# Kernel optimization log

Measured on AMD Instinct MI355X. Metric: run time of the kernel, lower is better.

The kernel has to match this reference:

```python
import jax, jax.numpy as jnp
import numpy as np

N = 100000      # nodes
E = 1600000     # edges
F_IN = 128      # node feature dim
F_E = 16        # edge feature dim
H = 4           # heads
C = 32          # per-head channels
NEG_SLOPE = 0.2


def setup_inputs() -> dict:
    key = jax.random.key(0)
    ks = jax.random.split(key, 8)
    s = 0.05
    x = jax.random.normal(ks[0], (N, F_IN), jnp.float32)
    edge_index = jax.random.randint(ks[1], (2, E), 0, N, jnp.int32)
    edge_attr = jax.random.normal(ks[2], (E, F_E), jnp.float32)
    Wl = jax.random.normal(ks[3], (F_IN, H * C), jnp.float32) * s   # lin_l (source)
    Wr = jax.random.normal(ks[4], (F_IN, H * C), jnp.float32) * s   # lin_r (target)
    We = jax.random.normal(ks[5], (F_E, H * C), jnp.float32) * s    # lin_edge
    att = jax.random.normal(ks[6], (H, C), jnp.float32) * s         # attention vector a
    bias = jnp.zeros((H * C,), jnp.float32)
    return {"x": x, "edge_index": edge_index, "edge_attr": edge_attr,
            "Wl": Wl, "Wr": Wr, "We": We, "att": att, "bias": bias}


def reference(x, edge_index, edge_attr, Wl, Wr, We, att, bias):
    n = x.shape[0]
    src, dst = edge_index[0], edge_index[1]

    # add_self_loops=True, fill_value='mean': self-loop edge_attr of node i is the
    # mean of edge_attr of edges whose destination is i (0 if no incoming edges).
    ea_sum = jax.ops.segment_sum(edge_attr, dst, num_segments=n)            # [n, Fe]
    cnt = jax.ops.segment_sum(jnp.ones((edge_attr.shape[0], 1), edge_attr.dtype),
                              dst, num_segments=n)                          # [n, 1]
    loop_attr = ea_sum / jnp.maximum(cnt, 1.0)
    loop = jnp.arange(n, dtype=src.dtype)
    src2 = jnp.concatenate([src, loop])                                     # [E+n]
    dst2 = jnp.concatenate([dst, loop])
    ea2 = jnp.concatenate([edge_attr, loop_attr], axis=0)                   # [E+n, Fe]

    # GATv2: score_e = att . leaky_relu(Wl x_src + Wr x_dst + We e)
    xl = (x @ Wl).reshape(n, H, C)
    xr = (x @ Wr).reshape(n, H, C)
    ee = (ea2 @ We).reshape(-1, H, C)
    e = jax.nn.leaky_relu(xl[src2] + xr[dst2] + ee, NEG_SLOPE)              # [E+n, H, C]
    logit = jnp.einsum('ehc,hc->eh', e, att)                                # [E+n, H]

    # segment softmax over destination node (self-loops guarantee nonempty segments)
    m = jax.ops.segment_max(logit, dst2, num_segments=n)                    # [n, H]
    ev = jnp.exp(logit - m[dst2])
    denom = jax.ops.segment_sum(ev, dst2, num_segments=n)
    alpha = ev / denom[dst2]                                                # [E+n, H]

    # scatter-aggregate weighted source messages
    out = jax.ops.segment_sum(alpha[:, :, None] * xl[src2], dst2, num_segments=n)
    out = out.reshape(n, H * C) + bias
    return jax.nn.relu(out), alpha
```

## Files before the change

kernel.cpp:

```cpp
#include <hip/hip_runtime.h>
#include <hip/hip_bf16.h>

#define HC   128
#define FE   16
#define NEG  0.2f
#define SPAD 140

using bf16 = __hip_bfloat16;
using f16  = _Float16;
typedef _Float16 h2 __attribute__((ext_vector_type(2)));
typedef short s16x8 __attribute__((ext_vector_type(8)));
typedef float f32x4 __attribute__((ext_vector_type(4)));

static __device__ __forceinline__ size_t szt(int a) { return (size_t)a; }
static __device__ __forceinline__ short b16rne(float f) {
    unsigned u = __float_as_uint(f);
    unsigned r = (u + 0x7fffu + ((u >> 16) & 1u)) >> 16;
    return (short)r;
}
static __device__ __forceinline__ unsigned pkh(float x, float y) {
    auto h = __builtin_amdgcn_cvt_pkrtz(x, y);
    return __builtin_bit_cast(unsigned, h);
}
static __device__ __forceinline__ float hlo(unsigned u) {
    h2 v = __builtin_bit_cast(h2, u); return (float)v.x;
}
static __device__ __forceinline__ float hhi(unsigned u) {
    h2 v = __builtin_bit_cast(h2, u); return (float)v.y;
}
static __device__ __forceinline__ float dot2(h2 a, h2 b, float c) {
#if __has_builtin(__builtin_amdgcn_fdot2)
    return __builtin_amdgcn_fdot2(a, b, c, false);
#else
    return c + (float)a.x * (float)b.x + (float)a.y * (float)b.y;
#endif
}
static __device__ __forceinline__ int xcc_id() {
    int x;
    asm volatile("s_getreg_b32 %0, hwreg(HW_REG_XCC_ID)" : "=s"(x));
    return x & 7;
}


__global__ void k_rank(const int* __restrict__ dst, int* __restrict__ cnt2,
                       int* __restrict__ rank, int E) {
    int g = xcc_id();
    int base = (blockIdx.x * 256 + threadIdx.x) * 4;
    if (base >= E) return;
    unsigned gtag = (unsigned)g << 28;
    if (base + 3 < E) {
        int4 d4 = *reinterpret_cast<const int4*>(dst + base);
        int r0 = __hip_atomic_fetch_add(&cnt2[d4.x * 8 + g], 1, __ATOMIC_RELAXED,
                                        __HIP_MEMORY_SCOPE_WORKGROUP);
        int r1 = __hip_atomic_fetch_add(&cnt2[d4.y * 8 + g], 1, __ATOMIC_RELAXED,
                                        __HIP_MEMORY_SCOPE_WORKGROUP);
        int r2 = __hip_atomic_fetch_add(&cnt2[d4.z * 8 + g], 1, __ATOMIC_RELAXED,
                                        __HIP_MEMORY_SCOPE_WORKGROUP);
        int r3 = __hip_atomic_fetch_add(&cnt2[d4.w * 8 + g], 1, __ATOMIC_RELAXED,
                                        __HIP_MEMORY_SCOPE_WORKGROUP);
        *reinterpret_cast<int4*>(rank + base) =
            make_int4(r0 | gtag, r1 | gtag, r2 | gtag, r3 | gtag);
    } else {
        for (int e = base; e < E; ++e) {
            int r = __hip_atomic_fetch_add(&cnt2[dst[e] * 8 + g], 1, __ATOMIC_RELAXED,
                                           __HIP_MEMORY_SCOPE_WORKGROUP);
            rank[e] = r | gtag;
        }
    }
}

__global__ __launch_bounds__(1024) void k_scan1(const int* __restrict__ cnt,
                                                int* __restrict__ excl,
                                                int* __restrict__ bsum, int n) {
    __shared__ int wsum[16];
    int t = threadIdx.x, lane = t & 63, wv = t >> 6;
    int i = blockIdx.x * 4096 + t * 4;
    int4 c = make_int4(0, 0, 0, 0);
    if (i + 3 < n) c = *reinterpret_cast<const int4*>(&cnt[i]);
    else if (i < n) {
        c.x = cnt[i];
        c.y = (i + 1 < n) ? cnt[i + 1] : 0;
        c.z = (i + 2 < n) ? cnt[i + 2] : 0;
    }
    int tot = c.x + c.y + c.z + c.w;
    int s = tot;
    #pragma unroll
    for (int d = 1; d < 64; d <<= 1) { int u = __shfl_up(s, d); if (lane >= d) s += u; }
    if (lane == 63) wsum[wv] = s;
    __syncthreads();
    if (t < 16) {
        int ws = wsum[t];
        #pragma unroll
        for (int d = 1; d < 16; d <<= 1) { int u = __shfl_up(ws, d); if (t >= d) ws += u; }
        wsum[t] = ws;
    }
    __syncthreads();
    int excl_t = (wv ? wsum[wv - 1] : 0) + (s - tot);
    if (i < n) {
        int4 ro;
        ro.x = excl_t;
        ro.y = ro.x + c.x;
        ro.z = ro.y + c.y;
        ro.w = ro.z + c.z;
        if (i + 3 < n) *reinterpret_cast<int4*>(&excl[i]) = ro;
        else {
            excl[i] = ro.x;
            if (i + 1 < n) excl[i + 1] = ro.y;
            if (i + 2 < n) excl[i + 2] = ro.z;
        }
    }
    if (t == 0) bsum[blockIdx.x] = wsum[15];
}

__global__ void k_scan2(int* __restrict__ bsum, int nb) {
    int t = threadIdx.x;
    int carry = 0;
    for (int base = 0; base < nb; base += 64) {
        int i = base + t;
        int v = (i < nb) ? bsum[i] : 0;
        int s = v;
        #pragma unroll
        for (int d = 1; d < 64; d <<= 1) { int u = __shfl_up(s, d); if (t >= d) s += u; }
        if (i < nb) bsum[i] = carry + s - v;
        carry += __shfl(s, 63);
    }
}

__global__ void k_scan3(const int* __restrict__ bsum, int* __restrict__ off2,
                        int* __restrict__ row_off, int n8, int E) {
    int i = blockIdx.x * 256 + threadIdx.x;
    if (i < n8) {
        int v = off2[i] + bsum[i >> 12];
        off2[i] = v;
        if ((i & 7) == 0) row_off[i >> 3] = v;
    } else if (i == n8) {
        row_off[n8 >> 3] = E;
    }
}

__global__ void k_fill(const int* __restrict__ src, const int* __restrict__ dst,
                       const int* __restrict__ rank, const int* __restrict__ off2,
                       int4* __restrict__ pairs4, int E) {
    int base = (blockIdx.x * 256 + threadIdx.x) * 4;
    if (base >= E) return;
    if (base + 3 < E) {
        int4 d4 = *reinterpret_cast<const int4*>(dst + base);
        int4 s4 = *reinterpret_cast<const int4*>(src + base);
        int4 k4 = *reinterpret_cast<const int4*>(rank + base);
        int p0 = off2[d4.x * 8 + (((unsigned)k4.x) >> 28)] + (k4.x & 0x0FFFFFFF);
        int p1 = off2[d4.y * 8 + (((unsigned)k4.y) >> 28)] + (k4.y & 0x0FFFFFFF);
        int p2 = off2[d4.z * 8 + (((unsigned)k4.z) >> 28)] + (k4.z & 0x0FFFFFFF);
        int p3 = off2[d4.w * 8 + (((unsigned)k4.w) >> 28)] + (k4.w & 0x0FFFFFFF);
        pairs4[p0] = make_int4(s4.x, base + 0, d4.x, 0);
        pairs4[p1] = make_int4(s4.y, base + 1, d4.y, 0);
        pairs4[p2] = make_int4(s4.z, base + 2, d4.z, 0);
        pairs4[p3] = make_int4(s4.w, base + 3, d4.w, 0);
    } else {
        for (int e = base; e < E; ++e) {
            int d = dst[e], k = rank[e];
            int pos = off2[d * 8 + (((unsigned)k) >> 28)] + (k & 0x0FFFFFFF);
            pairs4[pos] = make_int4(src[e], e, d, 0);
        }
    }
}


__global__ void k_wprep(const float* __restrict__ Wl, const float* __restrict__ Wr,
                        s16x8* __restrict__ Wcf) {
    int idx = blockIdx.x * 256 + threadIdx.x;
    if (idx >= 4096) return;
    int kt = idx >> 10, nt = (idx >> 6) & 15, lane = idx & 63;
    int col = nt * 16 + (lane & 15);
    const float* W = (col < HC) ? Wl : Wr;
    int c = (col < HC) ? col : col - HC;
    s16x8 v;
    #pragma unroll
    for (int j = 0; j < 8; ++j) {
        int k = kt * 32 + (lane >> 4) * 8 + j;
        v[j] = b16rne(W[k * HC + c]);
    }
    Wcf[idx] = v;
}

__global__ void k_wprep2(const float* __restrict__ We, s16x8* __restrict__ Wecf) {
    int idx = blockIdx.x * 256 + threadIdx.x;
    if (idx >= 512) return;
    int lane = idx & 63, g = lane >> 4;
    int ch = (idx >> 6) * 16 + (lane & 15);
    s16x8 v = {0, 0, 0, 0, 0, 0, 0, 0};
    if (g < 2) {
        #pragma unroll
        for (int j = 0; j < 8; ++j)
            v[j] = b16rne(We[(g * 8 + j) * HC + ch]);
    }
    Wecf[idx] = v;
}


__global__ __launch_bounds__(256) void k_gemm2(const float* __restrict__ x,
                                               const s16x8* __restrict__ Wcf,
                                               f16* __restrict__ xlh,
                                               f16* __restrict__ xrh, int n) {
    int t = threadIdx.x, lane = t & 63, w = t >> 6;
    int m0 = blockIdx.x * 16;
    int arow = m0 + (lane & 15);
    if (arow >= n) arow = n - 1;
    const float* xrow = x + szt(arow) * HC + (lane >> 4) * 8;

    f32x4 acc[4];
    #pragma unroll
    for (int nt = 0; nt < 4; ++nt) acc[nt] = (f32x4){0.f, 0.f, 0.f, 0.f};

    #pragma unroll
    for (int kt = 0; kt < 4; ++kt) {
        float4 a0 = *reinterpret_cast<const float4*>(xrow + kt * 32);
        float4 a1 = *reinterpret_cast<const float4*>(xrow + kt * 32 + 4);
        s16x8 af;
        af[0] = b16rne(a0.x); af[1] = b16rne(a0.y);
        af[2] = b16rne(a0.z); af[3] = b16rne(a0.w);
        af[4] = b16rne(a1.x); af[5] = b16rne(a1.y);
        af[6] = b16rne(a1.z); af[7] = b16rne(a1.w);
        #pragma unroll
        for (int nt = 0; nt < 4; ++nt) {
            s16x8 bf = Wcf[(kt * 16 + w * 4 + nt) * 64 + lane];
            acc[nt] = __builtin_amdgcn_mfma_f32_16x16x32_bf16(af, bf, acc[nt], 0, 0, 0);
        }
    }

    f16* O = (w < 2) ? xlh : xrh;
    int colb = (w & 1) * 64;
    #pragma unroll
    for (int nt = 0; nt < 4; ++nt) {
        int col = colb + nt * 16 + (lane & 15);
        #pragma unroll
        for (int q = 0; q < 4; ++q) {
            int r = m0 + (lane >> 4) * 4 + q;
            if (r < n) O[szt(r) * HC + col] = (f16)acc[nt][q];
        }
    }
}


__global__ __launch_bounds__(256) void k_self(
    const f16* __restrict__ xlh, const f16* __restrict__ xrh,
    const float* __restrict__ ea, const int4* __restrict__ pairs4,
    const int* __restrict__ row_off, const float* __restrict__ We,
    const float* __restrict__ att, float* __restrict__ exself, int n)
{
    int lane = threadIdx.x & 63, wv = threadIdx.x >> 6;
    int node = blockIdx.x * 4 + wv;
    if (node >= n) return;
    int beg = row_off[node], end = row_off[node + 1];
    int js = lane >> 2, fq = (lane & 3) * 4;
    float4 s4 = make_float4(0.f, 0.f, 0.f, 0.f);
    if (beg < end) {
        int last = end - 1;
        int p = beg + js;
        int e_cur = pairs4[(p <= last) ? p : last].y;
        for (; p < end + js; p += 16) {
            int pn = p + 16; if (pn > last) pn = last;
            int e_next = pairs4[pn].y;
            float4 v = *reinterpret_cast<const float4*>(ea + szt(e_cur) * FE + fq);
            if (p < end) { s4.x += v.x; s4.y += v.y; s4.z += v.z; s4.w += v.w; }
            e_cur = e_next;
        }
    }
    #pragma unroll
    for (int d = 4; d < 64; d <<= 1) {
        s4.x += __shfl_xor(s4.x, d);
        s4.y += __shfl_xor(s4.y, d);
        s4.z += __shfl_xor(s4.z, d);
        s4.w += __shfl_xor(s4.w, d);
    }
    int deg = end - beg;
    float invd = (deg > 0) ? 1.f / (float)deg : 0.f;
    float4 m4 = make_float4(s4.x * invd, s4.y * invd, s4.z * invd, s4.w * invd);

    int c0 = lane * 2, h = lane >> 4;
    float e0 = 0.f, e1 = 0.f;
    #pragma unroll
    for (int kp = 0; kp < FE; ++kp) {
        float a;
        switch (kp & 3) {
            case 0: a = __shfl(m4.x, kp >> 2); break;
            case 1: a = __shfl(m4.y, kp >> 2); break;
            case 2: a = __shfl(m4.z, kp >> 2); break;
            default: a = __shfl(m4.w, kp >> 2); break;
        }
        float2 w = *reinterpret_cast<const float2*>(We + kp * HC + c0);
        e0 += a * w.x;
        e1 += a * w.y;
    }
    unsigned xu = *reinterpret_cast<const unsigned*>(xlh + szt(node) * HC + c0);
    unsigned ru = *reinterpret_cast<const unsigned*>(xrh + szt(node) * HC + c0);
    float2 av = *reinterpret_cast<const float2*>(att + c0);
    float t0 = hlo(xu) + hlo(ru) + e0; t0 = t0 > 0.f ? t0 : NEG * t0;
    float t1 = hhi(xu) + hhi(ru) + e1; t1 = t1 > 0.f ? t1 : NEG * t1;
    float part = av.x * t0 + av.y * t1;
    part += __shfl_xor(part, 1);
    part += __shfl_xor(part, 2);
    part += __shfl_xor(part, 4);
    part += __shfl_xor(part, 8);
    float ex = __expf(part);
    if ((lane & 15) == 0) exself[szt(node) * 4 + h] = ex;
}


__global__ __launch_bounds__(256) void k_logit(
    const f16* __restrict__ xlh, const f16* __restrict__ xrh,
    const float* __restrict__ ea,
    const int4* __restrict__ pairs4,
    const s16x8* __restrict__ Wecf, const float* __restrict__ att,
    float* __restrict__ exe_csr, int E)
{
    __shared__ unsigned short sP[4][16][SPAD];
    int lane = threadIdx.x & 63, wv = threadIdx.x >> 6;
    int p0 = (blockIdx.x * 4 + wv) * 16;
    if (p0 >= E) return;
    unsigned short (*sPw)[SPAD] = sP[wv];

    int ei = lane & 15, g = lane >> 4;
    int p = p0 + ei; if (p >= E) p = E - 1;
    int4 pr = pairs4[p];

    s16x8 bfrag = {0, 0, 0, 0, 0, 0, 0, 0};
    if (g < 2) {
        const float* ear = ea + szt(pr.y) * FE + g * 8;
        float4 q0 = *reinterpret_cast<const float4*>(ear);
        float4 q1 = *reinterpret_cast<const float4*>(ear + 4);
        bfrag[0] = b16rne(q0.x); bfrag[1] = b16rne(q0.y);
        bfrag[2] = b16rne(q0.z); bfrag[3] = b16rne(q0.w);
        bfrag[4] = b16rne(q1.x); bfrag[5] = b16rne(q1.y);
        bfrag[6] = b16rne(q1.z); bfrag[7] = b16rne(q1.w);
    }
    #pragma unroll
    for (int mt = 0; mt < 8; ++mt) {
        f32x4 a = __builtin_amdgcn_mfma_f32_16x16x32_bf16(
            Wecf[mt * 64 + lane], bfrag, (f32x4){0.f, 0.f, 0.f, 0.f}, 0, 0, 0);
        *reinterpret_cast<uint2*>(&sPw[ei][mt * 16 + g * 4]) =
            make_uint2(pkh(a[0], a[1]), pkh(a[2], a[3]));
    }

    int l = lane & 15;
    int ch0 = l * 8;
    float4 av0 = *reinterpret_cast<const float4*>(att + ch0);
    float4 av1 = *reinterpret_cast<const float4*>(att + ch0 + 4);
    h2 ah0 = __builtin_bit_cast(h2, pkh(av0.x, av0.y));
    h2 ah1 = __builtin_bit_cast(h2, pkh(av0.z, av0.w));
    h2 ah2 = __builtin_bit_cast(h2, pkh(av1.x, av1.y));
    h2 ah3 = __builtin_bit_cast(h2, pkh(av1.z, av1.w));
    const h2 cneg = {(f16)NEG, (f16)NEG};
    int m = E - p0; if (m > 16) m = 16;
    #pragma unroll
    for (int k = 0; k < 4; ++k) {
        int j = k * 4 + g;
        int sj = __shfl(pr.x, j);
        int dj = __shfl(pr.z, j);
        uint4 xv = *reinterpret_cast<const uint4*>(xlh + szt(sj) * HC + ch0);
        uint4 rv = *reinterpret_cast<const uint4*>(xrh + szt(dj) * HC + ch0);
        uint4 ev = *reinterpret_cast<const uint4*>(&sPw[j][ch0]);
        h2 t0 = __builtin_bit_cast(h2, xv.x) + __builtin_bit_cast(h2, rv.x)
              + __builtin_bit_cast(h2, ev.x);
        h2 t1 = __builtin_bit_cast(h2, xv.y) + __builtin_bit_cast(h2, rv.y)
              + __builtin_bit_cast(h2, ev.y);
        h2 t2 = __builtin_bit_cast(h2, xv.z) + __builtin_bit_cast(h2, rv.z)
              + __builtin_bit_cast(h2, ev.z);
        h2 t3 = __builtin_bit_cast(h2, xv.w) + __builtin_bit_cast(h2, rv.w)
              + __builtin_bit_cast(h2, ev.w);
        t0 = __builtin_elementwise_max(t0, t0 * cneg);
        t1 = __builtin_elementwise_max(t1, t1 * cneg);
        t2 = __builtin_elementwise_max(t2, t2 * cneg);
        t3 = __builtin_elementwise_max(t3, t3 * cneg);
        float part = dot2(t0, ah0, 0.f);
        part = dot2(t1, ah1, part);
        part = dot2(t2, ah2, part);
        part = dot2(t3, ah3, part);
        part += __shfl_xor(part, 1);
        part += __shfl_xor(part, 2);
        if ((lane & 3) == 0 && j < m)
            exe_csr[szt(p0 + j) * 4 + (l >> 2)] = __expf(part);
    }
}


__global__ __launch_bounds__(256) void k_aggr(
    const f16* __restrict__ xlh, const float* __restrict__ exe_csr,
    const float* __restrict__ exself,
    const int4* __restrict__ pairs4, const int* __restrict__ row_off,
    const float* __restrict__ bias, float* __restrict__ out,
    float* __restrict__ alpha, int n, int E)
{
    int lane = threadIdx.x & 63, wv = threadIdx.x >> 6;
    int node = blockIdx.x * 4 + wv;
    if (node >= n) return;
    int j = lane >> 4, cg = lane & 15, cb = cg * 8, h = cg >> 2;
    int beg = row_off[node], end = row_off[node + 1];
    float acc[8];
    #pragma unroll
    for (int i = 0; i < 8; ++i) acc[i] = 0.f;
    float den = 0.f;

    if (beg < end) {
        int last = end - 1;
        int p0 = beg + j; if (p0 > last) p0 = last;
        int4 pr = pairs4[p0];
        float ex = exe_csr[szt(p0) * 4 + h];
        uint4 xv = *reinterpret_cast<const uint4*>(xlh + szt(pr.x) * HC + cb);
        for (int p = beg; p < end; p += 4) {
            int pn = p + 4 + j; if (pn > last) pn = last;
            int4 prN = pairs4[pn];
            float exN = exe_csr[szt(pn) * 4 + h];
            uint4 xvN = *reinterpret_cast<const uint4*>(xlh + szt(prN.x) * HC + cb);
            if (p + j < end) {
                den += ex;
                acc[0] += ex * hlo(xv.x); acc[1] += ex * hhi(xv.x);
                acc[2] += ex * hlo(xv.y); acc[3] += ex * hhi(xv.y);
                acc[4] += ex * hlo(xv.z); acc[5] += ex * hhi(xv.z);
                acc[6] += ex * hlo(xv.w); acc[7] += ex * hhi(xv.w);
            }
            pr = prN; ex = exN; xv = xvN;
        }
    }
    #pragma unroll
    for (int i = 0; i < 8; ++i) {
        acc[i] += __shfl_xor(acc[i], 16);
        acc[i] += __shfl_xor(acc[i], 32);
    }
    den += __shfl_xor(den, 16);
    den += __shfl_xor(den, 32);

    float exs = exself[szt(node) * 4 + h];
    uint4 xs = *reinterpret_cast<const uint4*>(xlh + szt(node) * HC + cb);
    den += exs;
    acc[0] += exs * hlo(xs.x); acc[1] += exs * hhi(xs.x);
    acc[2] += exs * hlo(xs.y); acc[3] += exs * hhi(xs.y);
    acc[4] += exs * hlo(xs.z); acc[5] += exs * hhi(xs.z);
    acc[6] += exs * hlo(xs.w); acc[7] += exs * hhi(xs.w);

    float inv = 1.f / den;
    if (j == 0) {
        float4 b0 = *reinterpret_cast<const float4*>(bias + cb);
        float4 b1 = *reinterpret_cast<const float4*>(bias + cb + 4);
        float4 o0, o1;
        o0.x = acc[0] * inv + b0.x; o0.x = o0.x > 0.f ? o0.x : 0.f;
        o0.y = acc[1] * inv + b0.y; o0.y = o0.y > 0.f ? o0.y : 0.f;
        o0.z = acc[2] * inv + b0.z; o0.z = o0.z > 0.f ? o0.z : 0.f;
        o0.w = acc[3] * inv + b0.w; o0.w = o0.w > 0.f ? o0.w : 0.f;
        o1.x = acc[4] * inv + b1.x; o1.x = o1.x > 0.f ? o1.x : 0.f;
        o1.y = acc[5] * inv + b1.y; o1.y = o1.y > 0.f ? o1.y : 0.f;
        o1.z = acc[6] * inv + b1.z; o1.z = o1.z > 0.f ? o1.z : 0.f;
        o1.w = acc[7] * inv + b1.w; o1.w = o1.w > 0.f ? o1.w : 0.f;
        *reinterpret_cast<float4*>(out + szt(node) * HC + cb) = o0;
        *reinterpret_cast<float4*>(out + szt(node) * HC + cb + 4) = o1;
        if ((cg & 3) == 0)
            alpha[szt(E + node) * 4 + h] = exs * inv;
    }
    float invh = __shfl(inv, 4 * (lane & 3));
    for (int pp = beg + (lane >> 2); pp < end; pp += 16) {
        int eid = pairs4[pp].y;
        alpha[szt(eid) * 4 + (lane & 3)] = exe_csr[szt(pp) * 4 + (lane & 3)] * invh;
    }
}


extern "C" void kernel_launch(void* const* d_in, const int* in_sizes, int n_in,
                              void* d_out, int out_size, void* d_ws, size_t ws_size,
                              hipStream_t stream) {
    const float* x    = (const float*)d_in[0];
    const int*   ei   = (const int*)d_in[1];
    const float* ea   = (const float*)d_in[2];
    const float* Wl   = (const float*)d_in[3];
    const float* Wr   = (const float*)d_in[4];
    const float* We   = (const float*)d_in[5];
    const float* att  = (const float*)d_in[6];
    const float* bias = (const float*)d_in[7];

    const int n = in_sizes[0] / HC;
    const int E = in_sizes[1] / 2;
    const int* src = ei;
    const int* dst = ei + E;
    const int n8 = n * 8;

    char* w = (char*)d_ws;
    size_t off = 0;
    auto alloc = [&](size_t bytes) -> char* {
        char* p = w + off;
        off += (bytes + 255) & ~(size_t)255;
        return p;
    };
    f16*   xlh     = (f16*)  alloc((size_t)n * HC * 2);
    f16*   xrh     = (f16*)  alloc((size_t)n * HC * 2);
    float* exe_csr = (float*)alloc((size_t)E * 4 * 4);
    float* exself  = (float*)alloc((size_t)n * 4 * 4);
    int*   cnt2    = (int*)  alloc((size_t)n8 * 4);
    int*   off2    = (int*)  alloc((size_t)n8 * 4);
    int*   row_off = (int*)  alloc((size_t)(n + 1) * 4);
    int*   rank    = (int*)  alloc((size_t)E * 4);
    int4*  pairs4  = (int4*) alloc((size_t)E * 16);
    s16x8* Wcf     = (s16x8*)alloc((size_t)4096 * 16);
    s16x8* Wecf    = (s16x8*)alloc((size_t)512 * 16);
    int    nb      = (n8 + 4095) / 4096;
    int*   bsum    = (int*)  alloc((size_t)nb * 4);
    (void)ws_size;

    float* out_p   = (float*)d_out;
    float* alpha_p = (float*)d_out + (size_t)n * HC;

    (void)hipMemsetAsync(cnt2, 0, (size_t)n8 * 4, stream);
    k_rank <<<(E / 4 + 255) / 256, 256, 0, stream>>>(dst, cnt2, rank, E);
    k_scan1<<<nb, 1024, 0, stream>>>(cnt2, off2, bsum, n8);
    k_scan2<<<1, 64, 0, stream>>>(bsum, nb);
    k_scan3<<<(n8 + 1 + 255) / 256, 256, 0, stream>>>(bsum, off2, row_off, n8, E);
    k_fill <<<(E / 4 + 255) / 256, 256, 0, stream>>>(src, dst, rank, off2, pairs4, E);
    k_wprep<<<16, 256, 0, stream>>>(Wl, Wr, Wcf);
    k_wprep2<<<2, 256, 0, stream>>>(We, Wecf);
    k_gemm2<<<(n + 15) / 16, 256, 0, stream>>>(x, Wcf, xlh, xrh, n);
    k_self <<<(n + 3) / 4, 256, 0, stream>>>(xlh, xrh, ea, pairs4, row_off, We, att,
                                             exself, n);
    k_logit<<<(E + 63) / 64, 256, 0, stream>>>(xlh, xrh, ea, pairs4,
                                               Wecf, att, exe_csr, E);
    k_aggr <<<(n + 3) / 4, 256, 0, stream>>>(xlh, exe_csr, exself, pairs4, row_off,
                                             bias, out_p, alpha_p, n, E);
}
```

Baseline: 462.5 us.

## Precompute bf16 edge attributes in k_rank and deepen aggregation prefetch

k_rank now converts edge_attr to bf16 once, during its streaming pass, and writes a compact copy. k_self and k_logit then do their random gathers on this half-size array instead of the fp32 one. The aggregation loop is also unrolled to handle two edge groups per iteration, putting more gather loads in flight. The costs are an extra 51 MB write plus a re-read of edge_attr in k_rank, and the self-loop mean is now computed from bf16-rounded attributes.

```diff
diff --git a/kernel.cpp b/kernel.cpp
--- a/kernel.cpp
+++ b/kernel.cpp
@@ -18,6 +18,11 @@
     unsigned r = (u + 0x7fffu + ((u >> 16) & 1u)) >> 16;
     return (short)r;
 }
+static __device__ __forceinline__ unsigned pkb(float x, float y) {
+    return ((unsigned)(unsigned short)b16rne(y) << 16) | (unsigned)(unsigned short)b16rne(x);
+}
+static __device__ __forceinline__ float blb(unsigned u) { return __uint_as_float(u << 16); }
+static __device__ __forceinline__ float bhb(unsigned u) { return __uint_as_float(u & 0xffff0000u); }
 static __device__ __forceinline__ unsigned pkh(float x, float y) {
     auto h = __builtin_amdgcn_cvt_pkrtz(x, y);
     return __builtin_bit_cast(unsigned, h);
@@ -42,12 +47,30 @@
 }
 
 
-__global__ void k_rank(const int* __restrict__ dst, int* __restrict__ cnt2,
-                       int* __restrict__ rank, int E) {
+__global__ void k_rank(const int* __restrict__ dst, const float4* __restrict__ ea_in,
+                       int* __restrict__ cnt2, int* __restrict__ rank,
+                       uint4* __restrict__ eabf, int E) {
     int g = xcc_id();
     int base = (blockIdx.x * 256 + threadIdx.x) * 4;
     if (base >= E) return;
     unsigned gtag = (unsigned)g << 28;
+    #pragma unroll
+    for (int u = 0; u < 4; ++u) {
+        int e = base + u;
+        if (e < E) {
+            float4 q0 = ea_in[szt(e) * 4 + 0];
+            float4 q1 = ea_in[szt(e) * 4 + 1];
+            float4 q2 = ea_in[szt(e) * 4 + 2];
+            float4 q3 = ea_in[szt(e) * 4 + 3];
+            uint4 lo, hi;
+            lo.x = pkb(q0.x, q0.y); lo.y = pkb(q0.z, q0.w);
+            lo.z = pkb(q1.x, q1.y); lo.w = pkb(q1.z, q1.w);
+            hi.x = pkb(q2.x, q2.y); hi.y = pkb(q2.z, q2.w);
+            hi.z = pkb(q3.x, q3.y); hi.w = pkb(q3.z, q3.w);
+            eabf[szt(e) * 2 + 0] = lo;
+            eabf[szt(e) * 2 + 1] = hi;
+        }
+    }
     if (base + 3 < E) {
         int4 d4 = *reinterpret_cast<const int4*>(dst + base);
         int r0 = __hip_atomic_fetch_add(&cnt2[d4.x * 8 + g], 1, __ATOMIC_RELAXED,
@@ -243,7 +266,7 @@
 
 __global__ __launch_bounds__(256) void k_self(
     const f16* __restrict__ xlh, const f16* __restrict__ xrh,
-    const float* __restrict__ ea, const int4* __restrict__ pairs4,
+    const uint2* __restrict__ eab2, const int4* __restrict__ pairs4,
     const int* __restrict__ row_off, const float* __restrict__ We,
     const float* __restrict__ att, float* __restrict__ exself, int n)
 {
@@ -251,7 +274,7 @@
     int node = blockIdx.x * 4 + wv;
     if (node >= n) return;
     int beg = row_off[node], end = row_off[node + 1];
-    int js = lane >> 2, fq = (lane & 3) * 4;
+    int js = lane >> 2, fq = lane & 3;
     float4 s4 = make_float4(0.f, 0.f, 0.f, 0.f);
     if (beg < end) {
         int last = end - 1;
@@ -260,8 +283,11 @@
         for (; p < end + js; p += 16) {
             int pn = p + 16; if (pn > last) pn = last;
             int e_next = pairs4[pn].y;
-            float4 v = *reinterpret_cast<const float4*>(ea + szt(e_cur) * FE + fq);
-            if (p < end) { s4.x += v.x; s4.y += v.y; s4.z += v.z; s4.w += v.w; }
+            uint2 v = eab2[szt(e_cur) * 4 + fq];
+            if (p < end) {
+                s4.x += blb(v.x); s4.y += bhb(v.x);
+                s4.z += blb(v.y); s4.w += bhb(v.y);
+            }
             e_cur = e_next;
         }
     }
@@ -308,7 +334,7 @@
 
 __global__ __launch_bounds__(256) void k_logit(
     const f16* __restrict__ xlh, const f16* __restrict__ xrh,
-    const float* __restrict__ ea,
+    const uint4* __restrict__ eabf,
     const int4* __restrict__ pairs4,
     const s16x8* __restrict__ Wecf, const float* __restrict__ att,
     float* __restrict__ exe_csr, int E)
@@ -324,15 +350,8 @@
     int4 pr = pairs4[p];
 
     s16x8 bfrag = {0, 0, 0, 0, 0, 0, 0, 0};
-    if (g < 2) {
-        const float* ear = ea + szt(pr.y) * FE + g * 8;
-        float4 q0 = *reinterpret_cast<const float4*>(ear);
-        float4 q1 = *reinterpret_cast<const float4*>(ear + 4);
-        bfrag[0] = b16rne(q0.x); bfrag[1] = b16rne(q0.y);
-        bfrag[2] = b16rne(q0.z); bfrag[3] = b16rne(q0.w);
-        bfrag[4] = b16rne(q1.x); bfrag[5] = b16rne(q1.y);
-        bfrag[6] = b16rne(q1.z); bfrag[7] = b16rne(q1.w);
-    }
+    if (g < 2)
+        bfrag = __builtin_bit_cast(s16x8, eabf[szt(pr.y) * 2 + g]);
     #pragma unroll
     for (int mt = 0; mt < 8; ++mt) {
         f32x4 a = __builtin_amdgcn_mfma_f32_16x16x32_bf16(
@@ -402,23 +421,38 @@
 
     if (beg < end) {
         int last = end - 1;
-        int p0 = beg + j; if (p0 > last) p0 = last;
-        int4 pr = pairs4[p0];
-        float ex = exe_csr[szt(p0) * 4 + h];
-        uint4 xv = *reinterpret_cast<const uint4*>(xlh + szt(pr.x) * HC + cb);
-        for (int p = beg; p < end; p += 4) {
-            int pn = p + 4 + j; if (pn > last) pn = last;
-            int4 prN = pairs4[pn];
-            float exN = exe_csr[szt(pn) * 4 + h];
-            uint4 xvN = *reinterpret_cast<const uint4*>(xlh + szt(prN.x) * HC + cb);
+        int pA = beg + j;     if (pA > last) pA = last;
+        int pB = beg + 4 + j; if (pB > last) pB = last;
+        int sA = pairs4[pA].x;
+        int sB = pairs4[pB].x;
+        float exA = exe_csr[szt(pA) * 4 + h];
+        float exB = exe_csr[szt(pB) * 4 + h];
+        uint4 xvA = *reinterpret_cast<const uint4*>(xlh + szt(sA) * HC + cb);
+        uint4 xvB = *reinterpret_cast<const uint4*>(xlh + szt(sB) * HC + cb);
+        for (int p = beg; p < end; p += 8) {
+            int pC = p + 8 + j;  if (pC > last) pC = last;
+            int pD = p + 12 + j; if (pD > last) pD = last;
+            int sC = pairs4[pC].x;
+            int sD = pairs4[pD].x;
+            float exC = exe_csr[szt(pC) * 4 + h];
+            float exD = exe_csr[szt(pD) * 4 + h];
+            uint4 xvC = *reinterpret_cast<const uint4*>(xlh + szt(sC) * HC + cb);
+            uint4 xvD = *reinterpret_cast<const uint4*>(xlh + szt(sD) * HC + cb);
             if (p + j < end) {
-                den += ex;
-                acc[0] += ex * hlo(xv.x); acc[1] += ex * hhi(xv.x);
-                acc[2] += ex * hlo(xv.y); acc[3] += ex * hhi(xv.y);
-                acc[4] += ex * hlo(xv.z); acc[5] += ex * hhi(xv.z);
-                acc[6] += ex * hlo(xv.w); acc[7] += ex * hhi(xv.w);
+                den += exA;
+                acc[0] += exA * hlo(xvA.x); acc[1] += exA * hhi(xvA.x);
+                acc[2] += exA * hlo(xvA.y); acc[3] += exA * hhi(xvA.y);
+                acc[4] += exA * hlo(xvA.z); acc[5] += exA * hhi(xvA.z);
+                acc[6] += exA * hlo(xvA.w); acc[7] += exA * hhi(xvA.w);
             }
-            pr = prN; ex = exN; xv = xvN;
+            if (p + 4 + j < end) {
+                den += exB;
+                acc[0] += exB * hlo(xvB.x); acc[1] += exB * hhi(xvB.x);
+                acc[2] += exB * hlo(xvB.y); acc[3] += exB * hhi(xvB.y);
+                acc[4] += exB * hlo(xvB.z); acc[5] += exB * hhi(xvB.z);
+                acc[6] += exB * hlo(xvB.w); acc[7] += exB * hhi(xvB.w);
+            }
+            exA = exC; exB = exD; xvA = xvC; xvB = xvD;
         }
     }
     #pragma unroll
@@ -497,6 +531,7 @@
     int*   row_off = (int*)  alloc((size_t)(n + 1) * 4);
     int*   rank    = (int*)  alloc((size_t)E * 4);
     int4*  pairs4  = (int4*) alloc((size_t)E * 16);
+    uint4* eabf    = (uint4*)alloc((size_t)E * 32);
     s16x8* Wcf     = (s16x8*)alloc((size_t)4096 * 16);
     s16x8* Wecf    = (s16x8*)alloc((size_t)512 * 16);
     int    nb      = (n8 + 4095) / 4096;
@@ -507,7 +542,8 @@
     float* alpha_p = (float*)d_out + (size_t)n * HC;
 
     (void)hipMemsetAsync(cnt2, 0, (size_t)n8 * 4, stream);
-    k_rank <<<(E / 4 + 255) / 256, 256, 0, stream>>>(dst, cnt2, rank, E);
+    k_rank <<<(E / 4 + 255) / 256, 256, 0, stream>>>(dst, (const float4*)ea, cnt2,
+                                                     rank, eabf, E);
     k_scan1<<<nb, 1024, 0, stream>>>(cnt2, off2, bsum, n8);
     k_scan2<<<1, 64, 0, stream>>>(bsum, nb);
     k_scan3<<<(n8 + 1 + 255) / 256, 256, 0, stream>>>(bsum, off2, row_off, n8, E);
@@ -515,9 +551,9 @@
     k_wprep<<<16, 256, 0, stream>>>(Wl, Wr, Wcf);
     k_wprep2<<<2, 256, 0, stream>>>(We, Wecf);
     k_gemm2<<<(n + 15) / 16, 256, 0, stream>>>(x, Wcf, xlh, xrh, n);
-    k_self <<<(n + 3) / 4, 256, 0, stream>>>(xlh, xrh, ea, pairs4, row_off, We, att,
-                                             exself, n);
-    k_logit<<<(E + 63) / 64, 256, 0, stream>>>(xlh, xrh, ea, pairs4,
+    k_self <<<(n + 3) / 4, 256, 0, stream>>>(xlh, xrh, (const uint2*)eabf, pairs4,
+                                             row_off, We, att, exself, n);
+    k_logit<<<(E + 63) / 64, 256, 0, stream>>>(xlh, xrh, eabf, pairs4,
                                                Wecf, att, exe_csr, E);
     k_aggr <<<(n + 3) / 4, 256, 0, stream>>>(xlh, exe_csr, exself, pairs4, row_off,
                                              bias, out_p, alpha_p, n, E);
```

After: 480.8 us. 3.9% more time.
